# Optimization experiments

Hardware: AMD Instinct MI355X
Metric: run time of the kernel (lower is better)

## Reference

```python
import jax, jax.numpy as jnp
import numpy as np

H, W = 256, 256
FRONT_K = 8
ALPHA_T = 1.0 / 255.0
EPS = 1e-8               # transmittance early-stop threshold (meta_f32[4])
BG = (0.0, 0.0, 0.0)     # background color
CHUNK = 128              # gaussians composited per scan step


def setup_inputs() -> dict:
    key = jax.random.key(0)
    k1, k2, k3, k4, k5, k6, k7 = jax.random.split(key, 7)
    B, G = 2, 8192
    # gaussian centers spread over the image plane
    means2d = jax.random.uniform(k1, (B, G, 2), jnp.float32) * jnp.array([W, H], jnp.float32)
    # positive-definite conics (inverse 2D covariance): a, c > 0, |b| < sqrt(a*c)
    a = 0.05 + 0.45 * jax.random.uniform(k2, (B, G), jnp.float32)
    c = 0.05 + 0.45 * jax.random.uniform(k3, (B, G), jnp.float32)
    b = 0.5 * (jax.random.uniform(k4, (B, G), jnp.float32) - 0.5) * jnp.sqrt(a * c)
    conics = jnp.stack([a, b, c], axis=-1)
    colors = jax.random.uniform(k5, (B, G, 3), jnp.float32)
    opacities = jax.random.uniform(k6, (B, G), jnp.float32)
    depths = jax.random.uniform(k7, (B, G), jnp.float32) * 10.0
    return {"means2d": means2d, "conics": conics, "colors": colors,
            "opacities": opacities, "depths": depths}


def _rasterize_one(means2d, conics, colors, opacities, depths):
    # depth sort (stable, front-to-back)
    perm = jnp.argsort(depths, stable=True)
    m = means2d[perm]      # [G,2]
    co = conics[perm]      # [G,3]
    col = colors[perm]     # [G,3]
    op = opacities[perm]   # [G]
    G = m.shape[0]
    n_chunks = G // CHUNK

    px = jnp.arange(W, dtype=jnp.float32) + 0.5  # pixel centers
    py = jnp.arange(H, dtype=jnp.float32) + 0.5
    bg = jnp.asarray(BG, jnp.float32)

    def step(carry, chunk):
        accum, T, count = carry                    # [H,W,3], [H,W], [H,W] int32
        mC, coC, colC, opC = chunk                 # [K,2],[K,3],[K,3],[K]
        dx = px[None, None, :] - mC[:, 0][:, None, None]   # [K,1,W]
        dy = py[None, :, None] - mC[:, 1][:, None, None]   # [K,H,1]
        a = coC[:, 0][:, None, None]
        b = coC[:, 1][:, None, None]
        c = coC[:, 2][:, None, None]
        sigma = 0.5 * (a * dx * dx + c * dy * dy) + b * dx * dy  # [K,H,W]
        alpha = jnp.minimum(opC[:, None, None] * jnp.exp(-sigma), 0.999)
        alpha = jnp.where((sigma >= 0.0) & (alpha >= ALPHA_T), alpha, 0.0)
        kept = (alpha > 0.0).astype(jnp.int32)
        # front_k: only the first FRONT_K contributing gaussians per pixel
        before = count[None] + jnp.cumsum(kept, axis=0) - kept
        alpha = jnp.where(before < FRONT_K, alpha, 0.0)
        kept = (alpha > 0.0).astype(jnp.int32)
        one_m = 1.0 - alpha
        cp = jnp.cumprod(one_m, axis=0)                              # [K,H,W]
        Tc = T[None] * jnp.concatenate([jnp.ones((1, H, W), alpha.dtype), cp[:-1]], 0)
        w = jnp.where(Tc > EPS, Tc * alpha, 0.0)                     # early-stop gate
        accum = accum + jnp.einsum('khw,kc->hwc', w, colC)
        T = T * cp[-1]
        count = count + jnp.sum(kept, axis=0)
        return (accum, T, count), None

    chunks = (m.reshape(n_chunks, CHUNK, 2),
              co.reshape(n_chunks, CHUNK, 3),
              col.reshape(n_chunks, CHUNK, 3),
              op.reshape(n_chunks, CHUNK))
    init = (jnp.zeros((H, W, 3), jnp.float32),
            jnp.ones((H, W), jnp.float32),
            jnp.zeros((H, W), jnp.int32))
    (accum, T, _), _ = jax.lax.scan(step, init, chunks)
    return accum + T[..., None] * bg


def reference(means2d, conics, colors, opacities, depths):
    return jax.vmap(_rasterize_one)(means2d, conics, colors, opacities, depths)
```

## Files before the change

### kernel.cpp

```cpp
#include <hip/hip_runtime.h>
#include <math.h>

#define GN 8192
#define BN 2
#define HN 256
#define WN 256
#define FRONT_K 8
#define EPS_T 1e-8f
#define ALPHA_T (1.0f / 255.0f)
#define TDIM 32
#define NTILE (TDIM * TDIM)
#define CAP 256

__global__ __launch_bounds__(64) void pgr_clear(unsigned* __restrict__ cur)
{
    cur[blockIdx.x * 64 + threadIdx.x] = 0u;
}

__global__ __launch_bounds__(64) void pgr_prep(
    const float* __restrict__ means2d, const float* __restrict__ conics,
    const float* __restrict__ colors, const float* __restrict__ opac,
    const float* __restrict__ depths,
    unsigned* __restrict__ cur, unsigned long long* __restrict__ kent,
    float4* __restrict__ recA, float4* __restrict__ recB,
    float* __restrict__ recC)
{
    const int p = threadIdx.x >> 3;
    const int q = threadIdx.x & 7;
    int g = blockIdx.x * 8 + p;
    int b = g >> 13, i = g & (GN - 1);
    float2 mxy = reinterpret_cast<const float2*>(means2d)[g];
    float mx = mxy.x, my = mxy.y;
    float ca = conics[3 * g], cb = conics[3 * g + 1], cc = conics[3 * g + 2];
    float r = colors[3 * g], g2 = colors[3 * g + 1], b3 = colors[3 * g + 2];
    float op = opac[g];
    float dep = depths[g];

    float s = (op > 0.f) ? (__logf(255.0f * op) + 1e-4f) : -1.0f;
    if (s < 0.f) return;
    float det = fmaxf(ca * cc - cb * cb, 1e-12f);
    float dxm = sqrtf(2.f * s * cc / det) + 0.02f;
    float dym = sqrtf(2.f * s * ca / det) + 0.02f;
    int x0 = (int)floorf(mx - dxm - 0.5f), x1 = (int)ceilf(mx + dxm - 0.5f);
    int y0 = (int)floorf(my - dym - 0.5f), y1 = (int)ceilf(my + dym - 0.5f);
    if (x1 < 0 || x0 > WN - 1 || y1 < 0 || y0 > HN - 1) return;
    x0 = max(x0, 0); x1 = min(x1, WN - 1);
    y0 = max(y0, 0); y1 = min(y1, HN - 1);
    int tx0 = x0 >> 3, tx1 = x1 >> 3, ty0 = y0 >> 3, ty1 = y1 >> 3;
    int nx = tx1 - tx0 + 1;
    int ntl = nx * (ty1 - ty0 + 1);

    unsigned long long key =
        ((unsigned long long)__float_as_uint(dep) << 13) | (unsigned)i;
    float4 A = make_float4(mx, my, ca, cb);
    float4 B = make_float4(cc, op, r, g2);

    for (int idx = q; idx < ntl; idx += 8) {
        int ty = idx / nx;
        int tx = idx - ty * nx;
        int t = b * NTILE + (ty0 + ty) * TDIM + (tx0 + tx);
        unsigned pos = atomicAdd(&cur[t], 1u);
        if (pos < CAP) {
            int sl = t * CAP + (int)pos;
            kent[sl] = key;
            recA[sl] = A;
            recB[sl] = B;
            recC[sl] = b3;
        }
    }
}

__device__ __forceinline__ int rank_of(const unsigned long long* s_key,
                                       unsigned long long k, int L)
{
    int rank = 0, j = 0;
    for (; j + 4 <= L; j += 4) {
        unsigned long long k0 = s_key[j], k1 = s_key[j + 1];
        unsigned long long k2 = s_key[j + 2], k3 = s_key[j + 3];
        rank += (int)(k0 < k) + (int)(k1 < k) + (int)(k2 < k) + (int)(k3 < k);
    }
    for (; j < L; ++j) rank += (int)(s_key[j] < k);
    return rank;
}

__global__ __launch_bounds__(256) void pgr_raster(
    const unsigned* __restrict__ cur, const unsigned long long* __restrict__ kent,
    const float4* __restrict__ recA, const float4* __restrict__ recB,
    const float* __restrict__ recC, float* __restrict__ out)
{
    const int b = blockIdx.z;
    const int t = b * NTILE + blockIdx.y * TDIM + blockIdx.x;
    const int tid = threadIdx.x;
    const int tx0 = blockIdx.x * 8, ty0 = blockIdx.y * 8;

    __shared__ unsigned long long s_key[CAP];
    __shared__ float4 s_d0[CAP], s_d1[CAP];
    __shared__ float s_d2[CAP];

    const int base = t * CAP;
    unsigned long long myk = kent[base + tid];
    float4 r0 = recA[base + tid];
    float4 r1 = recB[base + tid];
    float r2 = recC[base + tid];
    const int L = min((int)cur[t], CAP);

    if (tid < L) s_key[tid] = myk;
    __syncthreads();

    if (tid < L) {
        int rank = rank_of(s_key, myk, L);
        s_d0[rank] = r0; s_d1[rank] = r1; s_d2[rank] = r2;
    }
    __syncthreads();

    if (tid >= 64) return;

    const int lx = tid & 7, ly = tid >> 3;
    const float px = tx0 + lx + 0.5f, py = ty0 + ly + 0.5f;

    float accR = 0.f, accG = 0.f, accB = 0.f, T = 1.f;
    int count = 0;
    bool done = false;

    for (int i0 = 0; i0 < L; i0 += 8) {
        if (__all((int)done)) break;
        float alpha[8], colR[8], colG[8], colB[8];
        bool valid[8];
        #pragma unroll
        for (int k = 0; k < 8; ++k) {
            int idx = i0 + k;
            bool act = (idx < L) && !done;
            int ii = act ? idx : i0;
            float4 d0 = s_d0[ii];
            float4 d1 = s_d1[ii];
            float dx = __fsub_rn(px, d0.x);
            float dy = __fsub_rn(py, d0.y);
            float t1 = __fmul_rn(__fmul_rn(d0.z, dx), dx);
            float t2 = __fmul_rn(__fmul_rn(d1.x, dy), dy);
            float sigma = __fadd_rn(__fmul_rn(0.5f, __fadd_rn(t1, t2)),
                                    __fmul_rn(__fmul_rn(d0.w, dx), dy));
            bool v = act && sigma >= 0.f && sigma <= 5.55f;
            float al = v ? fminf(__fmul_rn(d1.y, __expf(-sigma)), 0.999f) : 0.f;
            valid[k] = v && (al >= ALPHA_T);
            alpha[k] = al;
            colR[k] = d1.z; colG[k] = d1.w; colB[k] = s_d2[ii];
        }
        #pragma unroll
        for (int k = 0; k < 8; ++k) {
            if (valid[k] && !done) {
                float al = alpha[k];
                if (T > EPS_T) {
                    float w = __fmul_rn(T, al);
                    accR += w * colR[k];
                    accG += w * colG[k];
                    accB += w * colB[k];
                }
                T = __fmul_rn(T, __fsub_rn(1.f, al));
                count++;
                if (count >= FRONT_K || T <= EPS_T) done = true;
            }
        }
    }

    int o = ((b * HN + (ty0 + ly)) * WN + (tx0 + lx)) * 3;
    out[o] = accR;
    out[o + 1] = accG;
    out[o + 2] = accB;
}

extern "C" void kernel_launch(void* const* d_in, const int* in_sizes, int n_in,
                              void* d_out, int out_size, void* d_ws, size_t ws_size,
                              hipStream_t stream) {
    const float* means2d = (const float*)d_in[0];
    const float* conics  = (const float*)d_in[1];
    const float* colors  = (const float*)d_in[2];
    const float* opac    = (const float*)d_in[3];
    const float* depths  = (const float*)d_in[4];
    float* out = (float*)d_out;

    const int NSLOT = BN * NTILE * CAP;
    float4*             recA = (float4*)d_ws;
    float4*             recB = recA + NSLOT;
    unsigned long long* kent = (unsigned long long*)(recB + NSLOT);
    float*              recC = (float*)(kent + NSLOT);
    unsigned*           cur  = (unsigned*)(recC + NSLOT);

    pgr_clear<<<(BN * NTILE) / 64, 64, 0, stream>>>(cur);
    pgr_prep<<<(BN * GN) / 8, 64, 0, stream>>>(means2d, conics, colors, opac,
                                               depths, cur, kent, recA, recB, recC);
    pgr_raster<<<dim3(TDIM, TDIM, BN), 256, 0, stream>>>(
        cur, kent, recA, recB, recC, out);
}
```

Baseline: 41.26 us.

## Store per-gaussian records once and bin only indices per tile

The prep kernel now writes each gaussian's packed data and sort key once to per-gaussian arrays, and each tile bin stores only a 32-bit gaussian index instead of a full 44-byte record copy. The raster kernel gathers the records through these indices. This removes the replicated per-tile writes in prep, which cuts scattered write traffic. In exchange, raster does indirect, uncoalesced gathers from global memory, though the per-gaussian arrays are small enough to likely stay cache-resident.

```diff
diff --git a/kernel.cpp b/kernel.cpp
--- a/kernel.cpp
+++ b/kernel.cpp
@@ -21,9 +21,9 @@
     const float* __restrict__ means2d, const float* __restrict__ conics,
     const float* __restrict__ colors, const float* __restrict__ opac,
     const float* __restrict__ depths,
-    unsigned* __restrict__ cur, unsigned long long* __restrict__ kent,
-    float4* __restrict__ recA, float4* __restrict__ recB,
-    float* __restrict__ recC)
+    float4* __restrict__ dat0, float4* __restrict__ dat1,
+    float* __restrict__ dat2, unsigned long long* __restrict__ kdat,
+    unsigned* __restrict__ cur, unsigned* __restrict__ ent)
 {
     const int p = threadIdx.x >> 3;
     const int q = threadIdx.x & 7;
@@ -35,6 +35,13 @@
     float r = colors[3 * g], g2 = colors[3 * g + 1], b3 = colors[3 * g + 2];
     float op = opac[g];
     float dep = depths[g];
+
+    if (q == 0) {
+        dat0[g] = make_float4(mx, my, ca, cb);
+        dat1[g] = make_float4(cc, op, r, g2);
+        dat2[g] = b3;
+        kdat[g] = ((unsigned long long)__float_as_uint(dep) << 13) | (unsigned)i;
+    }
 
     float s = (op > 0.f) ? (__logf(255.0f * op) + 1e-4f) : -1.0f;
     if (s < 0.f) return;
@@ -50,23 +57,12 @@
     int nx = tx1 - tx0 + 1;
     int ntl = nx * (ty1 - ty0 + 1);
 
-    unsigned long long key =
-        ((unsigned long long)__float_as_uint(dep) << 13) | (unsigned)i;
-    float4 A = make_float4(mx, my, ca, cb);
-    float4 B = make_float4(cc, op, r, g2);
-
     for (int idx = q; idx < ntl; idx += 8) {
         int ty = idx / nx;
         int tx = idx - ty * nx;
         int t = b * NTILE + (ty0 + ty) * TDIM + (tx0 + tx);
         unsigned pos = atomicAdd(&cur[t], 1u);
-        if (pos < CAP) {
-            int sl = t * CAP + (int)pos;
-            kent[sl] = key;
-            recA[sl] = A;
-            recB[sl] = B;
-            recC[sl] = b3;
-        }
+        if (pos < CAP) ent[t * CAP + (int)pos] = (unsigned)i;
     }
 }
 
@@ -84,27 +80,35 @@
 }
 
 __global__ __launch_bounds__(256) void pgr_raster(
-    const unsigned* __restrict__ cur, const unsigned long long* __restrict__ kent,
-    const float4* __restrict__ recA, const float4* __restrict__ recB,
-    const float* __restrict__ recC, float* __restrict__ out)
+    const float4* __restrict__ dat0, const float4* __restrict__ dat1,
+    const float* __restrict__ dat2, const unsigned long long* __restrict__ kdat,
+    const unsigned* __restrict__ cur, const unsigned* __restrict__ ent,
+    float* __restrict__ out)
 {
     const int b = blockIdx.z;
     const int t = b * NTILE + blockIdx.y * TDIM + blockIdx.x;
     const int tid = threadIdx.x;
     const int tx0 = blockIdx.x * 8, ty0 = blockIdx.y * 8;
+    const int bG = b * GN;
 
     __shared__ unsigned long long s_key[CAP];
     __shared__ float4 s_d0[CAP], s_d1[CAP];
     __shared__ float s_d2[CAP];
 
     const int base = t * CAP;
-    unsigned long long myk = kent[base + tid];
-    float4 r0 = recA[base + tid];
-    float4 r1 = recB[base + tid];
-    float r2 = recC[base + tid];
     const int L = min((int)cur[t], CAP);
 
-    if (tid < L) s_key[tid] = myk;
+    unsigned long long myk = 0;
+    float4 r0, r1;
+    float r2 = 0.f;
+    if (tid < L) {
+        int idx = bG + (int)ent[base + tid];
+        myk = kdat[idx];
+        r0 = dat0[idx];
+        r1 = dat1[idx];
+        r2 = dat2[idx];
+        s_key[tid] = myk;
+    }
     __syncthreads();
 
     if (tid < L) {
@@ -178,16 +182,18 @@
     const float* depths  = (const float*)d_in[4];
     float* out = (float*)d_out;
 
-    const int NSLOT = BN * NTILE * CAP;
-    float4*             recA = (float4*)d_ws;
-    float4*             recB = recA + NSLOT;
-    unsigned long long* kent = (unsigned long long*)(recB + NSLOT);
-    float*              recC = (float*)(kent + NSLOT);
-    unsigned*           cur  = (unsigned*)(recC + NSLOT);
+    const int BG = BN * GN;
+    float4*             dat0 = (float4*)d_ws;
+    float4*             dat1 = dat0 + BG;
+    float*              dat2 = (float*)(dat1 + BG);
+    unsigned long long* kdat = (unsigned long long*)(dat2 + BG);
+    unsigned*           cur  = (unsigned*)(kdat + BG);
+    unsigned*           ent  = cur + BN * NTILE;
 
     pgr_clear<<<(BN * NTILE) / 64, 64, 0, stream>>>(cur);
     pgr_prep<<<(BN * GN) / 8, 64, 0, stream>>>(means2d, conics, colors, opac,
-                                               depths, cur, kent, recA, recB, recC);
+                                               depths, dat0, dat1, dat2, kdat,
+                                               cur, ent);
     pgr_raster<<<dim3(TDIM, TDIM, BN), 256, 0, stream>>>(
-        cur, kent, recA, recB, recC, out);
+        dat0, dat1, dat2, kdat, cur, ent, out);
 }
```

Result: faster. 39.13 us (median of 2 runs) (-5.2%).
